# Kernel optimization log

Measured on AMD Instinct MI355X. Metric: run time of the kernel, lower is better.

## Reference

```python
import jax, jax.numpy as jnp
import numpy as np

N = 256      # doc_length
V = 300      # embed_dim
H = 256      # GRU hidden size
VOCAB = 50000
FC = 512     # fc_hiddim
B = 64
SIGMA = 0.95


def setup_inputs() -> dict:
    key = jax.random.key(0)
    ks = jax.random.split(key, 14)
    g = lambda k, sh, sc: (jax.random.normal(k, sh, jnp.float32) * sc)
    return {
        "x": jax.random.randint(ks[0], (B, 2, N), 0, VOCAB),
        "embed": g(ks[1], (VOCAB, V), 0.1),
        "W_ih_f": g(ks[2], (3 * H, V), 0.05),
        "W_hh_f": g(ks[3], (3 * H, H), 0.05),
        "b_ih_f": jnp.zeros((3 * H,), jnp.float32),
        "b_hh_f": jnp.zeros((3 * H,), jnp.float32),
        "W_ih_b": g(ks[4], (3 * H, V), 0.05),
        "W_hh_b": g(ks[5], (3 * H, H), 0.05),
        "b_ih_b": jnp.zeros((3 * H,), jnp.float32),
        "b_hh_b": jnp.zeros((3 * H,), jnp.float32),
        "fc1_w": g(ks[6], (FC, 8 * H), 0.02),
        "fc1_b": jnp.zeros((FC,), jnp.float32),
        "fc2_w": g(ks[7], (1, FC), 0.05),
        "fc2_b": jnp.zeros((1,), jnp.float32),
    }


def _gru_dir(x_seq, W_ih, W_hh, b_ih, b_hh):
    # x_seq: [B, N, V] -> outputs [B, N, H] (torch nn.GRU gate math)
    xg = jnp.einsum('bnv,gv->bng', x_seq, W_ih) + b_ih  # [B,N,3H]
    xg = jnp.moveaxis(xg, 1, 0)                          # [N,B,3H]
    h0 = jnp.zeros((x_seq.shape[0], H), x_seq.dtype)

    def step(h, xgt):
        hg = h @ W_hh.T + b_hh
        xr, xz, xn = jnp.split(xgt, 3, axis=-1)
        hr, hz, hn = jnp.split(hg, 3, axis=-1)
        r = jax.nn.sigmoid(xr + hr)
        z = jax.nn.sigmoid(xz + hz)
        n = jnp.tanh(xn + r * hn)
        h_new = (1.0 - z) * n + z * h
        return h_new, h_new

    _, hs = jax.lax.scan(step, h0, xg)
    return jnp.moveaxis(hs, 0, 1)  # [B,N,H]


def _bigru(x_seq, W_ih_f, W_hh_f, b_ih_f, b_hh_f, W_ih_b, W_hh_b, b_ih_b, b_hh_b):
    fwd = _gru_dir(x_seq, W_ih_f, W_hh_f, b_ih_f, b_hh_f)
    bwd = _gru_dir(x_seq[:, ::-1], W_ih_b, W_hh_b, b_ih_b, b_hh_b)[:, ::-1]
    return jnp.concatenate([fwd, bwd], axis=-1)  # [B,N,2H]


def _attend_pool(o2, dist_bias):
    # o2: [B,N,D]; scores: [B,N,N] with squared-distance bias
    scores = jnp.einsum('bnd,bmd->bnm', o2, o2) - dist_bias
    a = jax.nn.softmax(scores, axis=2)
    o5 = jnp.einsum('bnm,bmd->bnd', a, o2)
    # avg/max pool over sequence -> [B, 2D]
    return jnp.concatenate([o5.mean(axis=1), o5.max(axis=1)], axis=1)


def reference(x, embed, W_ih_f, W_hh_f, b_ih_f, b_hh_f,
              W_ih_b, W_hh_b, b_ih_b, b_hh_b,
              fc1_w, fc1_b, fc2_w, fc2_b):
    emb = embed[x]  # [B,2,N,V]
    i = jnp.arange(N, dtype=jnp.float32)
    dist_bias = ((i[:, None] - i[None, :]) ** 2) / SIGMA  # [N,N]

    feats = []
    for s in range(2):  # the two documents of the pair
        o2 = _bigru(emb[:, s], W_ih_f, W_hh_f, b_ih_f, b_hh_f,
                    W_ih_b, W_hh_b, b_ih_b, b_hh_b)
        feats.append(_attend_pool(o2, dist_bias))
    o8a, o8b = feats

    z = jnp.concatenate([jnp.abs(o8a - o8b), o8a * o8b], axis=1)  # [B, 8H]
    h = jax.nn.relu(z @ fc1_w.T + fc1_b)
    out = jax.nn.sigmoid(h @ fc2_w.T + fc2_b)
    return out.reshape(-1)
```

## Files before the change

### kernel.cpp

```cpp
#include <hip/hip_runtime.h>
#include <hip/hip_bf16.h>

typedef __hip_bfloat16 bf16;
typedef __bf16 bf16x8 __attribute__((ext_vector_type(8)));
typedef float f32x4 __attribute__((ext_vector_type(4)));

#define SEQ 256
#define NB  64
#define NV  300
#define NH  256
#define G3  768
#define D2  512
#define LOG2E  1.44269504f
#define LOG2E2 2.88539008f

__device__ __forceinline__ ushort f2bs(float f){ __bf16 t = (__bf16)f; return *(ushort*)&t; }
__device__ __forceinline__ float u2f(uint u){ return __uint_as_float(u); }

__device__ __forceinline__ float ex2(float x){
#if __has_builtin(__builtin_amdgcn_exp2f)
  return __builtin_amdgcn_exp2f(x);
#else
  return __exp2f(x);
#endif
}
__device__ __forceinline__ float rcp_(float x){
#if __has_builtin(__builtin_amdgcn_rcpf)
  return __builtin_amdgcn_rcpf(x);
#else
  return 1.0f/x;
#endif
}

__device__ __forceinline__ void mm16(const float (*As)[68], const float (*Bs)[68],
                                     float acc[4][4], int ty, int tx){
  #pragma unroll
  for (int kk=0;kk<16;kk++){
    const float4 a4 = *(const float4*)&As[kk][ty*4];
    const float4 b4 = *(const float4*)&Bs[kk][tx*4];
    const float ai[4] = {a4.x,a4.y,a4.z,a4.w};
    const float bj[4] = {b4.x,b4.y,b4.z,b4.w};
    #pragma unroll
    for (int i=0;i<4;i++)
      #pragma unroll
      for (int j=0;j<4;j++)
        acc[i][j] = fmaf(ai[i], bj[j], acc[i][j]);
  }
}

__global__ __launch_bounds__(320) void k_emb(const int* __restrict__ x,
                                             const float* __restrict__ embed,
                                             ushort* __restrict__ E){
  const int t = threadIdx.x;
  const int rsub = t / 80, c4 = t - rsub*80;
  const int row = blockIdx.x*4 + rsub;
  const int s = row >> 14, b = (row >> 8) & 63, n = row & 255;
  const int token = x[(b*2 + s)*SEQ + n];
  const int k = c4*4;
  float4 v = make_float4(0,0,0,0);
  if (k < NV) v = *(const float4*)(embed + (size_t)token*NV + k);
  ushort4 o;
  o.x = f2bs(v.x); o.y = f2bs(v.y); o.z = f2bs(v.z); o.w = f2bs(v.w);
  *(ushort4*)(E + (size_t)row*320 + k) = o;
}

__global__ __launch_bounds__(320) void k_wih(const float* __restrict__ Wf,
                                             const float* __restrict__ Wb,
                                             ushort* __restrict__ W16){
  const int t = threadIdx.x;
  const int rsub = t / 80, c4 = t - rsub*80;
  const int g = blockIdx.x*4 + rsub;
  const int dir = g >= G3;
  const int gw = g - dir*G3;
  const float* __restrict__ W = dir ? Wb : Wf;
  const int k = c4*4;
  float4 v = make_float4(0,0,0,0);
  if (k < NV) v = *(const float4*)(W + (size_t)gw*NV + k);
  ushort4 o;
  o.x = f2bs(v.x); o.y = f2bs(v.y); o.z = f2bs(v.z); o.w = f2bs(v.w);
  *(ushort4*)(W16 + (size_t)g*320 + k) = o;
}

__global__ __launch_bounds__(256) void k_wpk(const float* __restrict__ Wf,
                                             const float* __restrict__ Wb,
                                             ushort* __restrict__ wpk){
  const int idx = blockIdx.x*256 + threadIdx.x;
  const int l   = idx & 63;
  const int kf  = (idx >> 6) & 7;
  const int r2  = idx >> 9;
  const int tau = r2 % 3;
  const int r3  = r2 / 3;
  const int w   = r3 & 15;
  const int dir = r3 >> 4;
  const int g   = tau*256 + w*16 + (l & 15);
  const int kb  = kf*32 + (l >> 4)*8;
  const float sc = (tau < 2) ? LOG2E : LOG2E2;
  const float* __restrict__ W = dir ? Wb : Wf;
  #pragma unroll
  for (int e=0;e<8;e++)
    wpk[(size_t)idx*8 + e] = f2bs(W[(size_t)g*NH + kb + e] * sc);
}

__global__ __launch_bounds__(256) void k_xgm(const ushort* __restrict__ E,
    const ushort* __restrict__ W16,
    const float* __restrict__ bihf, const float* __restrict__ bihb,
    const float* __restrict__ bhhf, const float* __restrict__ bhhb,
    char* __restrict__ xgq)
{
  __shared__ __align__(16) char SM[34816];
  char* As = SM;
  char* Bs = SM + 10240;
  const int tid = threadIdx.x, w = tid >> 6, l = tid & 63, l15 = l & 15, lg = l >> 4;
  const int r0 = blockIdx.x * 128;
  const int c0 = blockIdx.y * 128;
  const int dir = (c0 >= G3);
  const int cw0 = c0 - dir*G3;
  const float* __restrict__ bih = dir ? bihb : bihf;
  const float* __restrict__ bhh = dir ? bhhb : bhhf;

  const int srow = tid >> 1, sc_ = (tid & 1)*32;
  f32x4 acc[2][8] = {};

  for (int ks = 0; ks < 10; ks++){
    const uint4 a0 = *(const uint4*)((const char*)E + (size_t)(r0+srow)*640 + ks*64 + sc_);
    const uint4 a1 = *(const uint4*)((const char*)E + (size_t)(r0+srow)*640 + ks*64 + sc_ + 16);
    const uint4 b0 = *(const uint4*)((const char*)W16 + (size_t)(c0+srow)*640 + ks*64 + sc_);
    const uint4 b1 = *(const uint4*)((const char*)W16 + (size_t)(c0+srow)*640 + ks*64 + sc_ + 16);
    __syncthreads();
    *(uint4*)&As[srow*80 + sc_] = a0;
    *(uint4*)&As[srow*80 + sc_ + 16] = a1;
    *(uint4*)&Bs[srow*80 + sc_] = b0;
    *(uint4*)&Bs[srow*80 + sc_ + 16] = b1;
    __syncthreads();
    bf16x8 am[2], bn[8];
    #pragma unroll
    for (int mm=0;mm<2;mm++) am[mm] = *(const bf16x8*)&As[(w*32 + mm*16 + l15)*80 + lg*16];
    #pragma unroll
    for (int nt=0;nt<8;nt++)  bn[nt] = *(const bf16x8*)&Bs[(nt*16 + l15)*80 + lg*16];
    #pragma unroll
    for (int mm=0;mm<2;mm++)
      #pragma unroll
      for (int nt=0;nt<8;nt++)
        acc[mm][nt] = __builtin_amdgcn_mfma_f32_16x16x32_bf16(am[mm], bn[nt], acc[mm][nt], 0,0,0);
  }

  __syncthreads();
  ushort* Cs = (ushort*)SM;
  #pragma unroll
  for (int nt=0;nt<8;nt++){
    const int cwb = cw0 + nt*16;
    const float sc2 = (cwb < 512) ? LOG2E : LOG2E2;
    const float bias = bih[cwb + l15] + ((cwb < 512) ? bhh[cwb + l15] : 0.0f);
    #pragma unroll
    for (int mm=0;mm<2;mm++)
      #pragma unroll
      for (int j=0;j<4;j++){
        const int row = w*32 + mm*16 + lg*4 + j;
        Cs[row*136 + nt*16 + l15] = f2bs((acc[mm][nt][j] + bias) * sc2);
      }
  }
  __syncthreads();
  const int tau = cw0 >> 8;
  const int u0  = cw0 & 255;
  #pragma unroll
  for (int i=0;i<8;i++){
    const int idx = i*256 + tid;
    const int row = idx >> 4, c16 = idx & 15;
    const int R = r0 + row;
    const int s_ = R >> 14, b_ = (R >> 8) & 63, n_ = R & 255;
    const int blk = (s_*2 + dir)*16 + (b_ >> 2);
    const uint4 v = *(const uint4*)&Cs[row*136 + c16*8];
    *(uint4*)(xgq + ((size_t)blk*256 + n_)*6144 + ((b_&3)*3 + tau)*512 + u0*2 + c16*16) = v;
  }
}

#define HSTR 544
__global__ __launch_bounds__(1024, 4) void k_gru(const char* __restrict__ xgq,
      const ushort* __restrict__ wpk,
      const float* __restrict__ bhhf, const float* __restrict__ bhhb,
      ushort* __restrict__ o2b)
{
  __shared__ __align__(16) char SMEM[2*16*HSTR];
  const int tid = threadIdx.x, w = tid >> 6, l = tid & 63, l15 = l & 15, lg = l >> 4;
  const int wgid = blockIdx.x;
  const int chain = wgid >> 4, sl = wgid & 15;
  const int s = chain >> 1, dir = chain & 1;
  const int sb64 = s*64 + sl*4;
  const float* __restrict__ bhh = dir ? bhhb : bhhf;
  const char* wbg = (const char*)wpk + (size_t)(dir*16 + w) * 24576;

  bf16x8 Wr[3][8];
  #pragma unroll
  for (int tau=0; tau<3; tau++)
    #pragma unroll
    for (int kf=0; kf<8; kf++)
      Wr[tau][kf] = *(const bf16x8*)(wbg + (size_t)((tau*8 + kf)*64 + l)*16);

  const float bn = bhh[512 + w*16 + l15] * LOG2E2;

  for (int k = tid; k < 4352; k += 1024) ((float*)SMEM)[k] = 0.0f;

  const int n0 = dir ? 255 : 0;
  const int qstep = dir ? -6144 : 6144;
  const int ostep = dir ? -1024 : 1024;
  const char* qb = xgq + ((size_t)wgid*256 + n0)*6144 + lg*1536 + (w*16 + l15)*2;
  char* op = (char*)o2b + ((size_t)(sb64 + lg)*256 + n0)*1024 + dir*512 + (w*16 + l15)*2;

  const int aoff = l15*HSTR + lg*16;
  const int hwoff = lg*4*HSTR + (w*16 + l15)*2;
  float hpv = 0.0f;

  __syncthreads();

  #pragma unroll 1
  for (int t=0; t<SEQ; t++){
    const int cur = t & 1;
    const int hcur = cur*8704, hnxt = (cur^1)*8704;

    const ushort q0 = *(const ushort*)(qb);
    const ushort q1 = *(const ushort*)(qb + 512);
    const ushort q2 = *(const ushort*)(qb + 1024);
    qb += qstep;

    f32x4 C[3] = {};
    #pragma unroll
    for (int kf=0; kf<8; kf++){
      const bf16x8 a = *(const bf16x8*)&SMEM[hcur + aoff + kf*64];
      C[0] = __builtin_amdgcn_mfma_f32_16x16x32_bf16(a, Wr[0][kf], C[0], 0, 0, 0);
      C[1] = __builtin_amdgcn_mfma_f32_16x16x32_bf16(a, Wr[1][kf], C[1], 0, 0, 0);
      C[2] = __builtin_amdgcn_mfma_f32_16x16x32_bf16(a, Wr[2][kf], C[2], 0, 0, 0);
    }

    const float xr = u2f((uint)q0 << 16);
    const float xz = u2f((uint)q1 << 16);
    const float xn = u2f((uint)q2 << 16);
    const float r  = rcp_(1.0f + ex2(-(xr + C[0][0])));
    const float z  = rcp_(1.0f + ex2(-(xz + C[1][0])));
    const float e2 = ex2(xn + r*(C[2][0] + bn));
    const float nn = (e2 - 1.0f) * rcp_(e2 + 1.0f);
    const float h  = nn + z*(hpv - nn);
    hpv = h;
    const ushort hs = f2bs(h);
    *(ushort*)&SMEM[hnxt + hwoff] = hs;
    *(ushort*)op = hs;
    op += ostep;
    __syncthreads();
  }
}

__global__ __launch_bounds__(256) void k_tr(const ushort* __restrict__ o2b,
                                            ushort* __restrict__ o2t){
  __shared__ __align__(16) char Ts[64*144];
  const int t = threadIdx.x;
  const int sb = blockIdx.z;
  const int n0 = blockIdx.x*64, d0 = blockIdx.y*64;
  const char* src = (const char*)o2b + (size_t)sb*262144;
  char* dst = (char*)o2t + (size_t)sb*262144;
  const int r = t >> 3, ch = t & 7;
  #pragma unroll
  for (int p=0;p<2;p++){
    const int row = r + p*32;
    const uint4 v = *(const uint4*)(src + (size_t)(n0+row)*1024 + d0*2 + ch*16);
    *(uint4*)&Ts[row*144 + ch*16] = v;
  }
  __syncthreads();
  #pragma unroll
  for (int p=0;p<2;p++){
    const int d = r + p*32;
    uint o[4];
    #pragma unroll
    for (int i=0;i<4;i++){
      const uint lo = *(const ushort*)&Ts[(ch*8 + 2*i)*144 + d*2];
      const uint hi = *(const ushort*)&Ts[(ch*8 + 2*i + 1)*144 + d*2];
      o[i] = lo | (hi << 16);
    }
    *(uint4*)(dst + (size_t)(d0+d)*512 + n0*2 + ch*16) = *(uint4*)o;
  }
}

__global__ __launch_bounds__(256) void k_scores(const ushort* __restrict__ o2b,
                                                float* __restrict__ sc){
  __shared__ __align__(16) char As[64*144];
  __shared__ __align__(16) char Bs[64*144];
  const int tid = threadIdx.x, w = tid >> 6, l = tid & 63, l15 = l & 15, lg = l >> 4;
  const int sb = blockIdx.z;
  const int n0 = blockIdx.x*64, m0 = blockIdx.y*64;
  const char* ob = (const char*)o2b + (size_t)sb*262144;
  const int srow = tid >> 2, scf = (tid & 3)*16;
  f32x4 acc[4] = {};
  for (int it=0; it<8; it++){
    const int k0 = it*64;
    const uint4 a0 = *(const uint4*)(ob + (size_t)(n0+srow)*1024 + k0*2 + scf);
    const uint4 a1 = *(const uint4*)(ob + (size_t)(n0+srow)*1024 + k0*2 + scf + 64);
    const uint4 b0 = *(const uint4*)(ob + (size_t)(m0+srow)*1024 + k0*2 + scf);
    const uint4 b1 = *(const uint4*)(ob + (size_t)(m0+srow)*1024 + k0*2 + scf + 64);
    __syncthreads();
    *(uint4*)&As[srow*144 + scf] = a0;
    *(uint4*)&As[srow*144 + scf + 64] = a1;
    *(uint4*)&Bs[srow*144 + scf] = b0;
    *(uint4*)&Bs[srow*144 + scf + 64] = b1;
    __syncthreads();
    #pragma unroll
    for (int ks=0; ks<2; ks++){
      const bf16x8 a = *(const bf16x8*)&As[(w*16 + l15)*144 + ks*64 + lg*16];
      #pragma unroll
      for (int nt=0; nt<4; nt++){
        const bf16x8 b = *(const bf16x8*)&Bs[(nt*16 + l15)*144 + ks*64 + lg*16];
        acc[nt] = __builtin_amdgcn_mfma_f32_16x16x32_bf16(a, b, acc[nt], 0, 0, 0);
      }
    }
  }
  #pragma unroll
  for (int nt=0; nt<4; nt++)
    #pragma unroll
    for (int j=0; j<4; j++){
      const int n = n0 + w*16 + lg*4 + j;
      const int m = m0 + nt*16 + l15;
      const float d = (float)(n - m);
      sc[((size_t)sb*SEQ + n)*SEQ + m] = acc[nt][j] - d*d*(1.0f/0.95f);
    }
}

__global__ __launch_bounds__(256) void k_softmax(const float* __restrict__ sc,
                                                 ushort* __restrict__ P){
  const int row = blockIdx.x*4 + (threadIdx.x >> 6);
  const int lane = threadIdx.x & 63;
  const float4 v = *(const float4*)(sc + (size_t)row*SEQ + lane*4);
  float m = fmaxf(fmaxf(v.x,v.y), fmaxf(v.z,v.w));
  #pragma unroll
  for (int off=32; off; off>>=1) m = fmaxf(m, __shfl_xor(m, off));
  float4 e;
  e.x = __expf(v.x-m); e.y = __expf(v.y-m); e.z = __expf(v.z-m); e.w = __expf(v.w-m);
  float ssum = e.x+e.y+e.z+e.w;
  #pragma unroll
  for (int off=32; off; off>>=1) ssum += __shfl_xor(ssum, off);
  const float inv = 1.0f/ssum;
  uint2 o;
  o.x = (uint)f2bs(e.x*inv) | ((uint)f2bs(e.y*inv) << 16);
  o.y = (uint)f2bs(e.z*inv) | ((uint)f2bs(e.w*inv) << 16);
  *(uint2*)((char*)P + (size_t)row*512 + lane*8) = o;
}

__global__ __launch_bounds__(256) void k_o5(const ushort* __restrict__ P,
                                            const ushort* __restrict__ o2t,
                                            ushort* __restrict__ o5b){
  __shared__ __align__(16) char As[64*144];
  __shared__ __align__(16) char Bs[64*144];
  const int tid = threadIdx.x, w = tid >> 6, l = tid & 63, l15 = l & 15, lg = l >> 4;
  const int sb = blockIdx.z;
  const int n0 = blockIdx.x*64, d0 = blockIdx.y*64;
  const char* pa = (const char*)P + (size_t)sb*131072;
  const char* pb = (const char*)o2t + (size_t)sb*262144;
  const int srow = tid >> 2, scf = (tid & 3)*16;
  f32x4 acc[4] = {};
  for (int it=0; it<4; it++){
    const int k0 = it*64;
    const uint4 a0 = *(const uint4*)(pa + (size_t)(n0+srow)*512 + k0*2 + scf);
    const uint4 a1 = *(const uint4*)(pa + (size_t)(n0+srow)*512 + k0*2 + scf + 64);
    const uint4 b0 = *(const uint4*)(pb + (size_t)(d0+srow)*512 + k0*2 + scf);
    const uint4 b1 = *(const uint4*)(pb + (size_t)(d0+srow)*512 + k0*2 + scf + 64);
    __syncthreads();
    *(uint4*)&As[srow*144 + scf] = a0;
    *(uint4*)&As[srow*144 + scf + 64] = a1;
    *(uint4*)&Bs[srow*144 + scf] = b0;
    *(uint4*)&Bs[srow*144 + scf + 64] = b1;
    __syncthreads();
    #pragma unroll
    for (int ks=0; ks<2; ks++){
      const bf16x8 a = *(const bf16x8*)&As[(w*16 + l15)*144 + ks*64 + lg*16];
      #pragma unroll
      for (int nt=0; nt<4; nt++){
        const bf16x8 b = *(const bf16x8*)&Bs[(nt*16 + l15)*144 + ks*64 + lg*16];
        acc[nt] = __builtin_amdgcn_mfma_f32_16x16x32_bf16(a, b, acc[nt], 0, 0, 0);
      }
    }
  }
  #pragma unroll
  for (int nt=0; nt<4; nt++)
    #pragma unroll
    for (int j=0; j<4; j++){
      const int n = n0 + w*16 + lg*4 + j;
      const int d = d0 + nt*16 + l15;
      *(ushort*)((char*)o5b + (size_t)sb*262144 + (size_t)n*1024 + d*2) = f2bs(acc[nt][j]);
    }
}

__global__ __launch_bounds__(256) void k_pool(const ushort* __restrict__ o5b,
                                              float* __restrict__ feats){
  const int idx = blockIdx.x*256 + threadIdx.x;
  const int sb = idx >> 9, d = idx & 511;
  const ushort* __restrict__ Pp = o5b + (size_t)sb*SEQ*D2 + d;
  float sum = 0.0f, mx = -1e30f;
  for (int n=0;n<SEQ;n++){
    const float v = u2f(((uint)Pp[(size_t)n*D2]) << 16);
    sum += v; mx = fmaxf(mx, v);
  }
  feats[(size_t)sb*1024 + d] = sum*(1.0f/256.0f);
  feats[(size_t)sb*1024 + 512 + d] = mx;
}

__global__ __launch_bounds__(256) void k_z(const float* __restrict__ feats,
                                           float* __restrict__ Z){
  const int idx = blockIdx.x*256 + threadIdx.x;
  const int b = idx >> 11, k = idx & 2047;
  const int j = (k < 1024) ? k : (k - 1024);
  const float fa = feats[(size_t)b*1024 + j];
  const float fb = feats[(size_t)(64 + b)*1024 + j];
  Z[idx] = (k < 1024) ? fabsf(fa - fb) : fa*fb;
}

__global__ __launch_bounds__(256) void k_fc1(const float* __restrict__ Z,
                                             const float* __restrict__ w,
                                             const float* __restrict__ bias,
                                             float* __restrict__ h1){
  __shared__ float As[16][68];
  __shared__ float Bs[16][68];
  const int tid = threadIdx.x;
  const int c0 = blockIdx.x*64;
  const int lr = tid >> 2, lk = (tid & 3)*4;
  const int ty = tid >> 4, tx = tid & 15;
  float acc[4][4] = {};
  for (int k0=0;k0<2048;k0+=16){
    const float4 a = *(const float4*)(Z + (size_t)lr*2048 + k0 + lk);
    const float4 b = *(const float4*)(w + (size_t)(c0+lr)*2048 + k0 + lk);
    __syncthreads();
    As[lk+0][lr]=a.x; As[lk+1][lr]=a.y; As[lk+2][lr]=a.z; As[lk+3][lr]=a.w;
    Bs[lk+0][lr]=b.x; Bs[lk+1][lr]=b.y; Bs[lk+2][lr]=b.z; Bs[lk+3][lr]=b.w;
    __syncthreads();
    mm16(As, Bs, acc, ty, tx);
  }
  #pragma unroll
  for (int i=0;i<4;i++)
    #pragma unroll
    for (int j=0;j<4;j++)
      h1[(size_t)(ty*4+i)*512 + c0+tx*4+j] = fmaxf(acc[i][j] + bias[c0+tx*4+j], 0.0f);
}

__global__ __launch_bounds__(256) void k_fc2(const float* __restrict__ h1,
                                             const float* __restrict__ w2,
                                             const float* __restrict__ b2,
                                             float* __restrict__ out){
  __shared__ float red[256];
  const int b = blockIdx.x, tid = threadIdx.x;
  float p = h1[(size_t)b*512 + tid]*w2[tid] + h1[(size_t)b*512 + 256 + tid]*w2[256 + tid];
  red[tid] = p; __syncthreads();
  for (int s2=128; s2; s2>>=1){ if (tid < s2) red[tid] += red[tid+s2]; __syncthreads(); }
  if (tid == 0) out[b] = 1.0f/(1.0f + __expf(-(red[0] + b2[0])));
}

extern "C" void kernel_launch(void* const* d_in, const int* in_sizes, int n_in,
                              void* d_out, int out_size, void* d_ws, size_t ws_size,
                              hipStream_t stream){
  const int*   x     = (const int*)d_in[0];
  const float* embed = (const float*)d_in[1];
  const float* Wihf  = (const float*)d_in[2];
  const float* Whhf  = (const float*)d_in[3];
  const float* bihf  = (const float*)d_in[4];
  const float* bhhf  = (const float*)d_in[5];
  const float* Wihb  = (const float*)d_in[6];
  const float* Whhb  = (const float*)d_in[7];
  const float* bihb  = (const float*)d_in[8];
  const float* bhhb  = (const float*)d_in[9];
  const float* fc1w  = (const float*)d_in[10];
  const float* fc1b  = (const float*)d_in[11];
  const float* fc2w  = (const float*)d_in[12];
  const float* fc2b  = (const float*)d_in[13];
  float* out = (float*)d_out;

  char* ws = (char*)d_ws;
  char*   xgq    = ws;
  ushort* o2t    = (ushort*)ws;
  float*  scores = (float*)(ws + 33554432);
  ushort* P      = (ushort*)(ws + 67108864);
  ushort* o5b    = (ushort*)(ws + 83886080);
  ushort* E      = (ushort*)(ws + 100663296);
  ushort* o2b    = (ushort*)(ws + 121634816);
  ushort* W16    = (ushort*)(ws + 155189248);
  ushort* Wpk    = (ushort*)(ws + 156172288);
  float*  feats  = (float*)(ws + 156958720);
  float*  Z      = (float*)(ws + 157483008);
  float*  h1     = (float*)(ws + 158007296);

  k_emb<<<8192, 320, 0, stream>>>(x, embed, E);
  k_wih<<<384, 320, 0, stream>>>(Wihf, Wihb, W16);
  k_wpk<<<192, 256, 0, stream>>>(Whhf, Whhb, Wpk);
  k_xgm<<<dim3(256, 12), 256, 0, stream>>>(E, W16, bihf, bihb, bhhf, bhhb, xgq);
  k_gru<<<64, 1024, 0, stream>>>(xgq, Wpk, bhhf, bhhb, o2b);
  k_tr<<<dim3(4, 8, 128), 256, 0, stream>>>(o2b, o2t);
  k_scores<<<dim3(4, 4, 128), 256, 0, stream>>>(o2b, scores);
  k_softmax<<<8192, 256, 0, stream>>>(scores, P);
  k_o5<<<dim3(4, 8, 128), 256, 0, stream>>>(P, o2t, o5b);
  k_pool<<<256, 256, 0, stream>>>(o5b, feats);
  k_z<<<512, 256, 0, stream>>>(feats, Z);
  k_fc1<<<8, 256, 0, stream>>>(Z, fc1w, fc1b, h1);
  k_fc2<<<64, 256, 0, stream>>>(h1, fc2w, fc2b, out);
}
```

Measured before the change: 551.8 us.

## Fuse sequence pooling into o5 GEMM epilogue and widen xgm column tile

The attention-output GEMM now reduces its accumulator tile to per-block partial sums and maxima in shared memory. This removes the bf16 o5 tensor write and the strided pool kernel, which is replaced by a small combine kernel. The input-gate GEMM tile is doubled to 256 columns so each A tile is reused across more columns, halving the grid. The tradeoffs are more accumulator registers in xgm and pooling done on fp32 values instead of bf16-rounded ones.

Measured after the change: 592.2 us. 1.07x slower.

```diff
diff --git a/kernel.cpp b/kernel.cpp
--- a/kernel.cpp
+++ b/kernel.cpp
@@ -112,65 +112,76 @@
   char* Bs = SM + 10240;
   const int tid = threadIdx.x, w = tid >> 6, l = tid & 63, l15 = l & 15, lg = l >> 4;
   const int r0 = blockIdx.x * 128;
-  const int c0 = blockIdx.y * 128;
+  const int c0 = blockIdx.y * 256;
   const int dir = (c0 >= G3);
   const int cw0 = c0 - dir*G3;
+  const int tau = cw0 >> 8;
+  const float sc2 = (tau < 2) ? LOG2E : LOG2E2;
   const float* __restrict__ bih = dir ? bihb : bihf;
   const float* __restrict__ bhh = dir ? bhhb : bhhf;
 
-  const int srow = tid >> 1, sc_ = (tid & 1)*32;
-  f32x4 acc[2][8] = {};
+  const int srow = tid >> 1, sca = (tid & 1)*32;
+  f32x4 acc[2][16] = {};
 
   for (int ks = 0; ks < 10; ks++){
-    const uint4 a0 = *(const uint4*)((const char*)E + (size_t)(r0+srow)*640 + ks*64 + sc_);
-    const uint4 a1 = *(const uint4*)((const char*)E + (size_t)(r0+srow)*640 + ks*64 + sc_ + 16);
-    const uint4 b0 = *(const uint4*)((const char*)W16 + (size_t)(c0+srow)*640 + ks*64 + sc_);
-    const uint4 b1 = *(const uint4*)((const char*)W16 + (size_t)(c0+srow)*640 + ks*64 + sc_ + 16);
-    __syncthreads();
-    *(uint4*)&As[srow*80 + sc_] = a0;
-    *(uint4*)&As[srow*80 + sc_ + 16] = a1;
-    *(uint4*)&Bs[srow*80 + sc_] = b0;
-    *(uint4*)&Bs[srow*80 + sc_ + 16] = b1;
-    __syncthreads();
-    bf16x8 am[2], bn[8];
+    const uint4 a0 = *(const uint4*)((const char*)E + (size_t)(r0+srow)*640 + ks*64 + sca);
+    const uint4 a1 = *(const uint4*)((const char*)E + (size_t)(r0+srow)*640 + ks*64 + sca + 16);
+    const uint4 b0 = *(const uint4*)((const char*)W16 + (size_t)(c0+tid)*640 + ks*64);
+    const uint4 b1 = *(const uint4*)((const char*)W16 + (size_t)(c0+tid)*640 + ks*64 + 16);
+    const uint4 b2 = *(const uint4*)((const char*)W16 + (size_t)(c0+tid)*640 + ks*64 + 32);
+    const uint4 b3 = *(const uint4*)((const char*)W16 + (size_t)(c0+tid)*640 + ks*64 + 48);
+    __syncthreads();
+    *(uint4*)&As[srow*80 + sca] = a0;
+    *(uint4*)&As[srow*80 + sca + 16] = a1;
+    *(uint4*)&Bs[tid*80 +  0] = b0;
+    *(uint4*)&Bs[tid*80 + 16] = b1;
+    *(uint4*)&Bs[tid*80 + 32] = b2;
+    *(uint4*)&Bs[tid*80 + 48] = b3;
+    __syncthreads();
+    bf16x8 am[2];
     #pragma unroll
     for (int mm=0;mm<2;mm++) am[mm] = *(const bf16x8*)&As[(w*32 + mm*16 + l15)*80 + lg*16];
     #pragma unroll
-    for (int nt=0;nt<8;nt++)  bn[nt] = *(const bf16x8*)&Bs[(nt*16 + l15)*80 + lg*16];
-    #pragma unroll
-    for (int mm=0;mm<2;mm++)
+    for (int h=0; h<2; h++){
+      bf16x8 bn[8];
       #pragma unroll
-      for (int nt=0;nt<8;nt++)
-        acc[mm][nt] = __builtin_amdgcn_mfma_f32_16x16x32_bf16(am[mm], bn[nt], acc[mm][nt], 0,0,0);
-  }
-
-  __syncthreads();
+      for (int q=0;q<8;q++) bn[q] = *(const bf16x8*)&Bs[((h*8+q)*16 + l15)*80 + lg*16];
+      #pragma unroll
+      for (int mm=0;mm<2;mm++)
+        #pragma unroll
+        for (int q=0;q<8;q++)
+          acc[mm][h*8+q] = __builtin_amdgcn_mfma_f32_16x16x32_bf16(am[mm], bn[q], acc[mm][h*8+q], 0,0,0);
+    }
+  }
+
   ushort* Cs = (ushort*)SM;
   #pragma unroll
-  for (int nt=0;nt<8;nt++){
-    const int cwb = cw0 + nt*16;
-    const float sc2 = (cwb < 512) ? LOG2E : LOG2E2;
-    const float bias = bih[cwb + l15] + ((cwb < 512) ? bhh[cwb + l15] : 0.0f);
-    #pragma unroll
-    for (int mm=0;mm<2;mm++)
+  for (int p=0; p<2; p++){
+    __syncthreads();
+    #pragma unroll
+    for (int q=0;q<8;q++){
+      const int nt = p*8 + q;
+      const int cwb = cw0 + nt*16;
+      const float bias = bih[cwb + l15] + ((tau < 2) ? bhh[cwb + l15] : 0.0f);
       #pragma unroll
-      for (int j=0;j<4;j++){
-        const int row = w*32 + mm*16 + lg*4 + j;
-        Cs[row*136 + nt*16 + l15] = f2bs((acc[mm][nt][j] + bias) * sc2);
-      }
-  }
-  __syncthreads();
-  const int tau = cw0 >> 8;
-  const int u0  = cw0 & 255;
-  #pragma unroll
-  for (int i=0;i<8;i++){
-    const int idx = i*256 + tid;
-    const int row = idx >> 4, c16 = idx & 15;
-    const int R = r0 + row;
-    const int s_ = R >> 14, b_ = (R >> 8) & 63, n_ = R & 255;
-    const int blk = (s_*2 + dir)*16 + (b_ >> 2);
-    const uint4 v = *(const uint4*)&Cs[row*136 + c16*8];
-    *(uint4*)(xgq + ((size_t)blk*256 + n_)*6144 + ((b_&3)*3 + tau)*512 + u0*2 + c16*16) = v;
+      for (int mm=0;mm<2;mm++)
+        #pragma unroll
+        for (int j=0;j<4;j++){
+          const int row = w*32 + mm*16 + lg*4 + j;
+          Cs[row*136 + q*16 + l15] = f2bs((acc[mm][nt][j] + bias) * sc2);
+        }
+    }
+    __syncthreads();
+    #pragma unroll
+    for (int i=0;i<8;i++){
+      const int idx = i*256 + tid;
+      const int row = idx >> 4, c16 = idx & 15;
+      const int R = r0 + row;
+      const int s_ = R >> 14, b_ = (R >> 8) & 63, n_ = R & 255;
+      const int blk = (s_*2 + dir)*16 + (b_ >> 2);
+      const uint4 v = *(const uint4*)&Cs[row*136 + c16*8];
+      *(uint4*)(xgq + ((size_t)blk*256 + n_)*6144 + ((b_&3)*3 + tau)*512 + p*256 + c16*16) = v;
+    }
   }
 }
 
@@ -343,7 +354,8 @@
 
 __global__ __launch_bounds__(256) void k_o5(const ushort* __restrict__ P,
                                             const ushort* __restrict__ o2t,
-                                            ushort* __restrict__ o5b){
+                                            float* __restrict__ psum,
+                                            float* __restrict__ pmax){
   __shared__ __align__(16) char As[64*144];
   __shared__ __align__(16) char Bs[64*144];
   const int tid = threadIdx.x, w = tid >> 6, l = tid & 63, l15 = l & 15, lg = l >> 4;
@@ -375,28 +387,43 @@
       }
     }
   }
-  #pragma unroll
-  for (int nt=0; nt<4; nt++)
-    #pragma unroll
-    for (int j=0; j<4; j++){
-      const int n = n0 + w*16 + lg*4 + j;
-      const int d = d0 + nt*16 + l15;
-      *(ushort*)((char*)o5b + (size_t)sb*262144 + (size_t)n*1024 + d*2) = f2bs(acc[nt][j]);
-    }
-}
-
-__global__ __launch_bounds__(256) void k_pool(const ushort* __restrict__ o5b,
-                                              float* __restrict__ feats){
+  __syncthreads();
+  float* Ss = (float*)As;
+  float* Ms = (float*)Bs;
+  const int wlg = w*4 + lg;
+  #pragma unroll
+  for (int nt=0; nt<4; nt++){
+    const float s4 = acc[nt][0] + acc[nt][1] + acc[nt][2] + acc[nt][3];
+    const float m4 = fmaxf(fmaxf(acc[nt][0], acc[nt][1]), fmaxf(acc[nt][2], acc[nt][3]));
+    Ss[wlg*64 + nt*16 + l15] = s4;
+    Ms[wlg*64 + nt*16 + l15] = m4;
+  }
+  __syncthreads();
+  if (tid < 64){
+    float s = 0.0f, m = -1e30f;
+    #pragma unroll
+    for (int k=0; k<16; k++){
+      s += Ss[k*64 + tid];
+      m = fmaxf(m, Ms[k*64 + tid]);
+    }
+    psum[((size_t)sb*4 + blockIdx.x)*512 + d0 + tid] = s;
+    pmax[((size_t)sb*4 + blockIdx.x)*512 + d0 + tid] = m;
+  }
+}
+
+__global__ __launch_bounds__(256) void k_poolc(const float* __restrict__ psum,
+                                               const float* __restrict__ pmax,
+                                               float* __restrict__ feats){
   const int idx = blockIdx.x*256 + threadIdx.x;
   const int sb = idx >> 9, d = idx & 511;
-  const ushort* __restrict__ Pp = o5b + (size_t)sb*SEQ*D2 + d;
-  float sum = 0.0f, mx = -1e30f;
-  for (int n=0;n<SEQ;n++){
-    const float v = u2f(((uint)Pp[(size_t)n*D2]) << 16);
-    sum += v; mx = fmaxf(mx, v);
-  }
-  feats[(size_t)sb*1024 + d] = sum*(1.0f/256.0f);
-  feats[(size_t)sb*1024 + 512 + d] = mx;
+  float s = 0.0f, m = -1e30f;
+  #pragma unroll
+  for (int nb=0; nb<4; nb++){
+    s += psum[((size_t)sb*4 + nb)*512 + d];
+    m = fmaxf(m, pmax[((size_t)sb*4 + nb)*512 + d]);
+  }
+  feats[(size_t)sb*1024 + d] = s*(1.0f/256.0f);
+  feats[(size_t)sb*1024 + 512 + d] = m;
 }
 
 __global__ __launch_bounds__(256) void k_z(const float* __restrict__ feats,
@@ -472,7 +499,8 @@
   ushort* o2t    = (ushort*)ws;
   float*  scores = (float*)(ws + 33554432);
   ushort* P      = (ushort*)(ws + 67108864);
-  ushort* o5b    = (ushort*)(ws + 83886080);
+  float*  psum   = (float*)(ws + 83886080);
+  float*  pmax   = (float*)(ws + 84934656);
   ushort* E      = (ushort*)(ws + 100663296);
   ushort* o2b    = (ushort*)(ws + 121634816);
   ushort* W16    = (ushort*)(ws + 155189248);
@@ -484,13 +512,13 @@
   k_emb<<<8192, 320, 0, stream>>>(x, embed, E);
   k_wih<<<384, 320, 0, stream>>>(Wihf, Wihb, W16);
   k_wpk<<<192, 256, 0, stream>>>(Whhf, Whhb, Wpk);
-  k_xgm<<<dim3(256, 12), 256, 0, stream>>>(E, W16, bihf, bihb, bhhf, bhhb, xgq);
+  k_xgm<<<dim3(256, 6), 256, 0, stream>>>(E, W16, bihf, bihb, bhhf, bhhb, xgq);
   k_gru<<<64, 1024, 0, stream>>>(xgq, Wpk, bhhf, bhhb, o2b);
   k_tr<<<dim3(4, 8, 128), 256, 0, stream>>>(o2b, o2t);
   k_scores<<<dim3(4, 4, 128), 256, 0, stream>>>(o2b, scores);
   k_softmax<<<8192, 256, 0, stream>>>(scores, P);
-  k_o5<<<dim3(4, 8, 128), 256, 0, stream>>>(P, o2t, o5b);
-  k_pool<<<256, 256, 0, stream>>>(o5b, feats);
+  k_o5<<<dim3(4, 8, 128), 256, 0, stream>>>(P, o2t, psum, pmax);
+  k_poolc<<<256, 256, 0, stream>>>(psum, pmax, feats);
   k_z<<<512, 256, 0, stream>>>(feats, Z);
   k_fc1<<<8, 256, 0, stream>>>(Z, fc1w, fc1b, h1);
   k_fc2<<<64, 256, 0, stream>>>(h1, fc2w, fc2b, out);
```
